# Optimization experiments

Measured on AMD Instinct MI355X. Metric: run time of the kernel, lower is better.

Reference implementation:

```python
import jax, jax.numpy as jnp
import numpy as np

B, NG, C, H = 16, 1024, 768, 12
CAP = 16  # fixed routing capacity in gpu_pair (8 box slots from 0 up, 8 cls slots from 15 down)


def layernorm(x, g, b, eps=1e-5):
    m = x.mean(-1, keepdims=True)
    v = jnp.mean((x - m) ** 2, axis=-1, keepdims=True)
    return (x - m) * jax.lax.rsqrt(v + eps) * g + b


def setup_inputs() -> dict:
    key = jax.random.key(0)
    ks = jax.random.split(key, 8)
    s = 0.02
    return {
        "general_token": jax.random.normal(ks[0], (B, NG, C), jnp.float32),
        "cls_token": jax.random.normal(ks[1], (B, 1, C), jnp.float32),
        "box_token": jax.random.normal(ks[2], (B, 1, C), jnp.float32),
        "w_qkv": jax.random.normal(ks[3], (3 * C, C), jnp.float32) * s,
        "w_proj": jax.random.normal(ks[4], (C, C), jnp.float32) * s,
        "b_proj": jnp.zeros((C,), jnp.float32),
        "gamma1": jnp.ones((C,), jnp.float32),
        "beta1": jnp.zeros((C,), jnp.float32),
    }


def _route(sum_a, is_box):
    """On-device replication of gpu_pair's serial CPU loop for slots 0..15.

    Tokens are processed in descending sum_attn order; box-preferred tokens fill
    slots 0,1,2,..., cls-preferred tokens fill slots 15,14,13,.... Each category's
    writer per slot is unique; on a box/cls collision the later (larger sorted
    position) write wins, matching the serial loop's overwrite semantics. Slots
    never written stay 0 (np.zeros init). Wrapped-around writes (rank >= 16) land
    outside slots 0..15 in the original and are irrelevant to the output.
    """
    ng = sum_a.shape[0]
    perm = jnp.argsort(-sum_a)                      # descending sort
    ib = is_box[perm]
    ibi = ib.astype(jnp.int32)
    box_rank = jnp.cumsum(ibi) - ibi                # exclusive prefix count of box tokens
    cls_rank = jnp.cumsum(1 - ibi) - (1 - ibi)      # exclusive prefix count of cls tokens
    j = jnp.arange(ng, dtype=jnp.int32)
    box_pos = jnp.where(ib & (box_rank < CAP), box_rank, CAP)
    cls_pos = jnp.where((~ib) & (cls_rank < CAP), (CAP - 1) - cls_rank, CAP)
    empty = jnp.full((CAP,), -1, jnp.int32)
    box_j = empty.at[box_pos].set(j, mode='drop')   # unique writer per slot
    cls_j = empty.at[cls_pos].set(j, mode='drop')
    win = jnp.maximum(box_j, cls_j)
    return jnp.where(win >= 0, perm[jnp.maximum(win, 0)], 0)


def reference(general_token, cls_token, box_token, w_qkv, w_proj, b_proj, gamma1, beta1):
    # cat order in torch: cat(cls, cat(box, general)) -> [cls, box, general]
    cat = jnp.concatenate([cls_token, box_token, general_token], axis=1)  # [B,N,C]
    Bq, N, Cq = cat.shape
    hd = Cq // H
    x = layernorm(cat, gamma1, beta1)
    qkv = (x @ w_qkv.T).reshape(Bq, N, 3, H, hd).transpose(2, 0, 3, 1, 4)
    q, k, v = qkv[0], qkv[1], qkv[2]
    attn = jnp.einsum('bhnd,bhmd->bhnm', q, k) * (hd ** -0.5)
    # raw scores between cls<->box zeroed BEFORE softmax (not -inf)
    attn = attn.at[:, :, 0, 1].set(0.0).at[:, :, 1, 0].set(0.0)
    attn = jax.nn.softmax(attn, axis=-1)
    out = jnp.einsum('bhnm,bhmd->bhnd', attn, v).transpose(0, 2, 1, 3).reshape(Bq, N, Cq)
    out = out @ w_proj.T + b_proj
    cat = cat + out  # residual (drop_path identity in eval)
    cls_t, box_t, gen = cat[:, 0:1], cat[:, 1:2], cat[:, 2:]
    cls_attn = attn[:, :, 0, 2:].mean(axis=1)  # [B, N-2]
    box_attn = attn[:, :, 1, 2:].mean(axis=1)
    idx = jax.vmap(_route)(cls_attn + box_attn, box_attn > cls_attn)  # [B,16]
    gathered = jnp.take_along_axis(gen, idx[:, :, None], axis=1)      # [B,16,C]
    cls_task_token = jnp.concatenate([cls_t, gathered[:, 0:8]], axis=1)   # [B,9,C]
    box_task_token = jnp.concatenate([box_t, gathered[:, 8:16]], axis=1)  # [B,9,C]
    return cls_task_token, box_task_token
```

## Files before the change

kernel.cpp:

```cpp
#include <hip/hip_runtime.h>
#include <math.h>

namespace {

constexpr int Bn = 16;
constexpr int NG = 1024;
constexpr int Cc = 768;
constexpr int Hh = 12;
constexpr int HD = 64;
constexpr int Nn = 1026;
constexpr int NR = 18;
constexpr int NPK = 1152;
constexpr int NCH = 8;

typedef __attribute__((ext_vector_type(8))) short short8;
typedef __attribute__((ext_vector_type(4))) float f32x4;

__device__ inline unsigned short f2bf(float f) {
  unsigned u = __float_as_uint(f);
  unsigned r = u + 0x7FFFu + ((u >> 16) & 1u);
  return (unsigned short)(r >> 16);
}

__global__ __launch_bounds__(256) void k_ln(
    const float* __restrict__ gen, const float* __restrict__ cls,
    const float* __restrict__ box, const float* __restrict__ gamma,
    const float* __restrict__ beta, float* __restrict__ x,
    unsigned short* __restrict__ xbf) {
  int blk = blockIdx.x;
  int b = blk / Nn, n = blk % Nn;
  const float* src = (n == 0) ? cls + (size_t)b * Cc
                   : (n == 1) ? box + (size_t)b * Cc
                              : gen + ((size_t)b * NG + (n - 2)) * Cc;
  int t = threadIdx.x;
  float v0 = src[t], v1 = src[t + 256], v2 = src[t + 512];
  __shared__ double red[8];
  double s = (double)v0 + (double)v1 + (double)v2;
  for (int o = 32; o > 0; o >>= 1) s += __shfl_down(s, o, 64);
  int wid = t >> 6, lid = t & 63;
  if (lid == 0) red[wid] = s;
  __syncthreads();
  if (t == 0) red[4] = (red[0] + red[1] + red[2] + red[3]) / Cc;
  __syncthreads();
  double mean = red[4];
  double d0 = (double)v0 - mean, d1 = (double)v1 - mean, d2 = (double)v2 - mean;
  double sq = d0 * d0 + d1 * d1 + d2 * d2;
  for (int o = 32; o > 0; o >>= 1) sq += __shfl_down(sq, o, 64);
  __syncthreads();
  if (lid == 0) red[wid] = sq;
  __syncthreads();
  if (t == 0) {
    double var = (red[0] + red[1] + red[2] + red[3]) / Cc;
    red[5] = 1.0 / sqrt(var + 1e-5);
  }
  __syncthreads();
  double rs = red[5];
  float* dst = x + ((size_t)b * Nn + n) * Cc;
  unsigned short* dbf = xbf + ((size_t)b * NPK + n) * Cc;
  float o0 = (float)(d0 * rs * (double)gamma[t]       + (double)beta[t]);
  float o1 = (float)(d1 * rs * (double)gamma[t + 256] + (double)beta[t + 256]);
  float o2 = (float)(d2 * rs * (double)gamma[t + 512] + (double)beta[t + 512]);
  dst[t] = o0; dst[t + 256] = o1; dst[t + 512] = o2;
  dbf[t] = f2bf(o0); dbf[t + 256] = f2bf(o1); dbf[t + 512] = f2bf(o2);
}

__global__ __launch_bounds__(256) void k_padzero(unsigned short* __restrict__ xbf) {
  constexpr int PERB = (NPK - Nn) * Cc / 2;
  int idx = blockIdx.x * 256 + threadIdx.x;
  int total = Bn * PERB;
  for (int i = idx; i < total; i += gridDim.x * 256) {
    int b = i / PERB, r = i % PERB;
    unsigned int* p = (unsigned int*)(xbf + ((size_t)b * NPK + Nn) * Cc);
    p[r] = 0u;
  }
}

__global__ __launch_bounds__(256) void k_xt(
    const unsigned short* __restrict__ xbf, unsigned short* __restrict__ xT) {
  int b = blockIdx.x, jt = blockIdx.y, ct = blockIdx.z;
  int j0 = jt * 64, c0 = ct * 64;
  __shared__ unsigned short ts[64][80];
  int t = threadIdx.x;
  #pragma unroll
  for (int l = 0; l < 2; l++) {
    int chunk = t + l * 256;
    int r = chunk >> 3, c8 = chunk & 7;
    uint4 v = *(const uint4*)(xbf + ((size_t)b * NPK + j0 + r) * Cc + c0 + c8 * 8);
    *(uint4*)&ts[r][c8 * 8] = v;
  }
  __syncthreads();
  #pragma unroll
  for (int l = 0; l < 2; l++) {
    int chunk = t + l * 256;
    int orow = chunk >> 3, j8 = chunk & 7;
    unsigned short tmp[8];
    #pragma unroll
    for (int i = 0; i < 8; i++) tmp[i] = ts[j8 * 8 + i][orow];
    *(uint4*)(xT + ((size_t)b * Cc + c0 + orow) * NPK + j0 + j8 * 8) = *(uint4*)tmp;
  }
}

__global__ __launch_bounds__(256) void k_wcvt(
    const float* __restrict__ wqkv, const float* __restrict__ wproj,
    unsigned short* __restrict__ wqb, unsigned short* __restrict__ wvb,
    unsigned short* __restrict__ wpb) {
  int i = (blockIdx.x * 256 + threadIdx.x) * 4;
  if (i >= Cc * Cc) return;
  const float* wq = wqkv;
  const float* wv = wqkv + (size_t)2 * Cc * Cc;
  float4 q = *(const float4*)(wq + i);
  float4 a = *(const float4*)(wv + i);
  float4 b = *(const float4*)(wproj + i);
  ushort4 oq, oa, ob;
  oq.x = f2bf(q.x); oq.y = f2bf(q.y); oq.z = f2bf(q.z); oq.w = f2bf(q.w);
  oa.x = f2bf(a.x); oa.y = f2bf(a.y); oa.z = f2bf(a.z); oa.w = f2bf(a.w);
  ob.x = f2bf(b.x); ob.y = f2bf(b.y); ob.z = f2bf(b.z); ob.w = f2bf(b.w);
  *(ushort4*)(wqb + i) = oq;
  *(ushort4*)(wvb + i) = oa;
  *(ushort4*)(wpb + i) = ob;
}

__global__ __launch_bounds__(256) void k_wkt(
    const float* __restrict__ wqkv, unsigned short* __restrict__ wkTb) {
  int rt = blockIdx.x, ct = blockIdx.y;
  __shared__ unsigned short ts[64][72];
  int t = threadIdx.x;
  const float* src = wqkv + (size_t)Cc * Cc;
  #pragma unroll
  for (int l = 0; l < 4; l++) {
    int idx = t + l * 256;
    int r = idx >> 4, c4 = idx & 15;
    float4 v = *(const float4*)(src + (size_t)(rt * 64 + r) * Cc + ct * 64 + c4 * 4);
    ts[r][c4 * 4 + 0] = f2bf(v.x); ts[r][c4 * 4 + 1] = f2bf(v.y);
    ts[r][c4 * 4 + 2] = f2bf(v.z); ts[r][c4 * 4 + 3] = f2bf(v.w);
  }
  __syncthreads();
  #pragma unroll
  for (int l = 0; l < 2; l++) {
    int idx = t + l * 256;
    int r2 = idx >> 3, j8 = idx & 7;
    unsigned short tmp[8];
    #pragma unroll
    for (int i = 0; i < 8; i++) tmp[i] = ts[j8 * 8 + i][r2];
    *(uint4*)(wkTb + (size_t)(ct * 64 + r2) * Cc + rt * 64 + j8 * 8) = *(uint4*)tmp;
  }
}

__global__ __launch_bounds__(256) void k_q01(
    const float* __restrict__ wqkv, const float* __restrict__ x,
    double* __restrict__ q01d) {
  int row = blockIdx.x;
  int b = row >> 1, i = row & 1;
  __shared__ float xl[Cc];
  const float* xr = x + ((size_t)b * Nn + i) * Cc;
  for (int c = threadIdx.x; c < Cc; c += 256) xl[c] = xr[c];
  __syncthreads();
  int w = threadIdx.x >> 6, lane = threadIdx.x & 63;
  int o = blockIdx.y * 4 + w;
  const float* wr = wqkv + (size_t)o * Cc + lane * 12;
  const float* xs = xl + lane * 12;
  double acc = 0;
  #pragma unroll
  for (int k = 0; k < 12; k++) acc += (double)wr[k] * (double)xs[k];
  for (int off = 32; off > 0; off >>= 1) acc += __shfl_down(acc, off, 64);
  if (lane == 0) q01d[(size_t)row * Cc + o] = acc;
}

__global__ __launch_bounds__(256) void k_u01(
    const float* __restrict__ wqkv, const double* __restrict__ q01d,
    double* __restrict__ u01d) {
  int blk = blockIdx.x;
  int h = blk % Hh; int i = (blk / Hh) & 1; int b = blk / (2 * Hh);
  __shared__ double qh[HD];
  const double* q = q01d + ((size_t)b * 2 + i) * Cc + h * HD;
  if (threadIdx.x < HD) qh[threadIdx.x] = q[threadIdx.x];
  __syncthreads();
  const float* wk = wqkv + (size_t)Cc * Cc;
  int c = blockIdx.y * 256 + threadIdx.x;
  double a0 = 0, a1 = 0, a2 = 0, a3 = 0;
  #pragma unroll 4
  for (int d = 0; d < HD; d += 4) {
    a0 += qh[d]     * (double)wk[(size_t)(h * HD + d) * Cc + c];
    a1 += qh[d + 1] * (double)wk[(size_t)(h * HD + d + 1) * Cc + c];
    a2 += qh[d + 2] * (double)wk[(size_t)(h * HD + d + 2) * Cc + c];
    a3 += qh[d + 3] * (double)wk[(size_t)(h * HD + d + 3) * Cc + c];
  }
  u01d[(((size_t)(b * 2 + i)) * Hh + h) * Cc + c] = (a0 + a1) + (a2 + a3);
}

__global__ __launch_bounds__(256) void k_rlogits(
    const double* __restrict__ u01d, const float* __restrict__ x,
    double* __restrict__ Ldp) {
  int b = blockIdx.x, jt = blockIdx.y, cch = blockIdx.z;
  int j0 = jt * 256;
  int t = threadIdx.x;
  int pl = t & 127;
  int g  = t >> 7;
  __shared__ float xtT[32][256];
  __shared__ double ut[24][32];
  double acc[12][2] = {};
  int cbase = cch * 96;
  for (int c0 = cbase; c0 < cbase + 96; c0 += 32) {
    {
      int j = j0 + t;
      if (j < Nn) {
        const float* xr = x + ((size_t)b * Nn + j) * Cc + c0;
        #pragma unroll
        for (int k = 0; k < 32; k += 4) {
          float4 v = *(const float4*)(xr + k);
          xtT[k][t] = v.x; xtT[k + 1][t] = v.y; xtT[k + 2][t] = v.z; xtT[k + 3][t] = v.w;
        }
      } else {
        for (int k = 0; k < 32; k++) xtT[k][t] = 0.f;
      }
    }
    for (int idx = t; idx < 24 * 32; idx += 256) {
      int r = idx >> 5, cc = idx & 31;
      ut[r][cc] = u01d[(((size_t)(b * 2 + (r / 12))) * Hh + (r % 12)) * Cc + c0 + cc];
    }
    __syncthreads();
    for (int cc = 0; cc < 32; cc++) {
      float2 xv = *(const float2*)&xtT[cc][pl * 2];
      double x0 = (double)xv.x, x1 = (double)xv.y;
      #pragma unroll
      for (int h = 0; h < 12; h++) {
        double uv = ut[g * 12 + h][cc];
        acc[h][0] += uv * x0;
        acc[h][1] += uv * x1;
      }
    }
    __syncthreads();
  }
  for (int h = 0; h < 12; h++) {
    #pragma unroll
    for (int k = 0; k < 2; k++) {
      int j = j0 + pl * 2 + k;
      if (j < Nn) {
        Ldp[(((size_t)cch * Bn + b) * 24 + g * 12 + h) * Nn + j] = acc[h][k] * 0.125;
      }
    }
  }
}

__global__ __launch_bounds__(256) void k_rsoftmax(
    const double* __restrict__ Ldp, double* __restrict__ Ld,
    unsigned short* __restrict__ Pb) {
  int blk = blockIdx.x;
  int h = blk % Hh; int i = (blk / Hh) & 1; int b = blk / (2 * Hh);
  double* row = Ld + (size_t)blk * Nn;
  unsigned short* prow = Pb + ((size_t)b * 216 + i * Hh + h) * NPK;
  int t = threadIdx.x;
  size_t poff = ((size_t)b * 24 + i * 12 + h) * Nn;
  constexpr size_t PSTRIDE = (size_t)Bn * 24 * Nn;
  double lv[5];
  int cnt = 0;
  double mx = -1e300;
  for (int j = t; j < Nn; j += 256) {
    double L = 0;
    #pragma unroll
    for (int p = 0; p < NCH; p++) L += Ldp[(size_t)p * PSTRIDE + poff + j];
    if (i == 0 && j == 1) L = 0.0;
    if (i == 1 && j == 0) L = 0.0;
    lv[cnt++] = L;
    mx = fmax(mx, L);
  }
  __shared__ double sd[256];
  sd[t] = mx; __syncthreads();
  for (int st = 128; st > 0; st >>= 1) { if (t < st) sd[t] = fmax(sd[t], sd[t + st]); __syncthreads(); }
  mx = sd[0]; __syncthreads();
  double sum = 0;
  for (int k = 0; k < cnt; k++) { lv[k] = exp(lv[k] - mx); sum += lv[k]; }
  sd[t] = sum; __syncthreads();
  for (int st = 128; st > 0; st >>= 1) { if (t < st) sd[t] += sd[t + st]; __syncthreads(); }
  double inv = 1.0 / sd[0];
  int k = 0;
  for (int j = t; j < Nn; j += 256) {
    double p = lv[k++] * inv;
    row[j] = p;
    prow[j] = f2bf((float)p);
  }
  for (int j = Nn + t; j < NPK; j += 256) prow[j] = 0;
}

__global__ __launch_bounds__(256) void k_rsums(
    const double* __restrict__ Ld, double* __restrict__ suma,
    double* __restrict__ diffd) {
  int b = blockIdx.x;
  for (int jg = threadIdx.x; jg < NG; jg += 256) {
    int j = jg + 2;
    double cs = 0, bs = 0;
    for (int h = 0; h < Hh; h++) {
      cs += Ld[(((size_t)(b * 2 + 0)) * Hh + h) * Nn + j];
      bs += Ld[(((size_t)(b * 2 + 1)) * Hh + h) * Nn + j];
    }
    cs /= 12.0; bs /= 12.0;
    suma[(size_t)b * NG + jg] = cs + bs;
    diffd[(size_t)b * NG + jg] = bs - cs;
  }
}

__global__ __launch_bounds__(256) void k_route(
    const double* __restrict__ suma, const double* __restrict__ diffd,
    int* __restrict__ rowcat) {
  int b = blockIdx.x, t = threadIdx.x;
  __shared__ double vals[NG];
  __shared__ unsigned char flags[NG];
  __shared__ double redv[4];
  __shared__ int redi[4];
  __shared__ int blist[16], clist[16];
  __shared__ double blv[16], clv[16];
  for (int j = t; j < NG; j += 256) {
    vals[j] = suma[(size_t)b * NG + j];
    flags[j] = diffd[(size_t)b * NG + j] > 0.0 ? 1 : 0;
  }
  __syncthreads();
  int half = t >> 7;
  int lt = t & 127;
  int wv = t >> 6;
  int lane = t & 63;
  for (int s = 0; s < 16; s++) {
    double bv = -1e300; int bi = 0x7fffffff;
    #pragma unroll
    for (int k = 0; k < 8; k++) {
      int j = lt * 8 + k;
      double v = vals[j];
      if (flags[j] == half && v > bv) { bv = v; bi = j; }
    }
    for (int off = 32; off > 0; off >>= 1) {
      double ov = __shfl_down(bv, off, 64);
      int oi = __shfl_down(bi, off, 64);
      if (ov > bv || (ov == bv && oi < bi)) { bv = ov; bi = oi; }
    }
    if (lane == 0) { redv[wv] = bv; redi[wv] = bi; }
    __syncthreads();
    if (lt == 0) {
      double v0 = redv[half * 2], v1 = redv[half * 2 + 1];
      int i0 = redi[half * 2], i1 = redi[half * 2 + 1];
      if (v1 > v0 || (v1 == v0 && i1 < i0)) { v0 = v1; i0 = i1; }
      int win = (v0 > -1e299) ? i0 : -1;
      if (half) { blist[s] = win; blv[s] = v0; }
      else      { clist[s] = win; clv[s] = v0; }
      if (win >= 0) vals[win] = -1e300;
    }
    __syncthreads();
  }
  if (t < 16) {
    int s = t;
    int bc = blist[s];
    int cl = clist[15 - s];
    double bvv = blv[s], cvv = clv[15 - s];
    int win;
    if (bc < 0 && cl < 0) win = -1;
    else if (bc < 0) win = cl;
    else if (cl < 0) win = bc;
    else {
      bool boxwins = (bvv < cvv) || (bvv == cvv && bc > cl);
      win = boxwins ? bc : cl;
    }
    int tok = (win >= 0) ? win : 0;
    rowcat[b * NR + 2 + s] = tok + 2;
  }
  if (t == 0) { rowcat[b * NR + 0] = 0; rowcat[b * NR + 1] = 1; }
}

__global__ __launch_bounds__(256) void k_qg_mfma(
    const unsigned short* __restrict__ xbf, const unsigned short* __restrict__ wqb,
    const int* __restrict__ rowcat, unsigned short* __restrict__ qb) {
  int mt = blockIdx.x, ng = blockIdx.y;
  int wid = threadIdx.x >> 6, lane = threadIdx.x & 63;
  int nt = ng * 4 + wid;
  int m = lane & 15, kg = lane >> 4;
  int rowi = mt * 16 + m;
  int b = rowi >> 4, s = rowi & 15;
  int tok = rowcat[b * NR + 2 + s];
  const unsigned short* abase = xbf + ((size_t)b * NPK + tok) * Cc + kg * 8;
  const unsigned short* bbase = wqb + (size_t)(nt * 16 + m) * Cc + kg * 8;
  f32x4 acc = {0, 0, 0, 0};
  for (int k0 = 0; k0 < Cc; k0 += 32) {
    short8 a = *(const short8*)(abase + k0);
    short8 bf = *(const short8*)(bbase + k0);
    acc = __builtin_amdgcn_mfma_f32_16x16x32_bf16(a, bf, acc, 0, 0, 0);
  }
  int c = nt * 16 + m;
  #pragma unroll
  for (int r = 0; r < 4; r++) {
    int rowo = mt * 16 + kg * 4 + r;
    qb[(size_t)rowo * Cc + c] = f2bf(acc[r]);
  }
}

__global__ __launch_bounds__(256) void k_ug_mfma(
    const unsigned short* __restrict__ qb, const unsigned short* __restrict__ wkTb,
    unsigned short* __restrict__ u16b) {
  int h = blockIdx.x, mt = blockIdx.y, ngz = blockIdx.z;
  int wid = threadIdx.x >> 6, lane = threadIdx.x & 63;
  int m = lane & 15, kg = lane >> 4;
  int rowi = mt * 16 + m;
  const unsigned short* abase = qb + (size_t)rowi * Cc + h * HD + kg * 8;
  f32x4 acc[4] = {{0,0,0,0},{0,0,0,0},{0,0,0,0},{0,0,0,0}};
  #pragma unroll
  for (int k0 = 0; k0 < HD; k0 += 32) {
    short8 a = *(const short8*)(abase + k0);
    #pragma unroll
    for (int t = 0; t < 4; t++) {
      int c = ngz * 256 + (wid * 4 + t) * 16 + m;
      short8 bf = *(const short8*)(wkTb + (size_t)c * Cc + h * HD + kg * 8 + k0);
      acc[t] = __builtin_amdgcn_mfma_f32_16x16x32_bf16(a, bf, acc[t], 0, 0, 0);
    }
  }
  #pragma unroll
  for (int t = 0; t < 4; t++) {
    int c = ngz * 256 + (wid * 4 + t) * 16 + m;
    #pragma unroll
    for (int r = 0; r < 4; r++) {
      int row = mt * 16 + kg * 4 + r;
      int b = row >> 4, s = row & 15;
      u16b[((size_t)b * 192 + s * Hh + h) * Cc + c] = f2bf(acc[t][r]);
    }
  }
}

__global__ __launch_bounds__(256) void k_glogits_mfma(
    const unsigned short* __restrict__ u16b, const unsigned short* __restrict__ xbf,
    float* __restrict__ S) {
  int b = blockIdx.x, mg = blockIdx.y, nz = blockIdx.z;
  __shared__ __align__(16) unsigned short Bs[2][128 * 32];
  int t = threadIdx.x, w = t >> 6, lane = t & 63;
  int wm = w >> 1, wn = w & 1;
  int m = lane & 15, kg = lane >> 4;
  int r0 = mg * 64 + wm * 32 + m;
  const unsigned short* a0p = u16b + ((size_t)b * 192 + r0) * Cc + kg * 8;
  const unsigned short* a1p = a0p + (size_t)16 * Cc;
  int scol = lane >> 2;
  int skp = (lane & 3) * 8;
  const unsigned short* gB0 = xbf + ((size_t)b * NPK + nz * 128 + w * 32 + scol) * Cc + skp;
  const unsigned short* gB1 = gB0 + (size_t)16 * Cc;
  int lo0 = (w * 32 + scol) * 32 + skp;
  int lo1 = lo0 + 16 * 32;
  constexpr int NIT = Cc / 32;
  short8 s0 = *(const short8*)(gB0);
  short8 s1 = *(const short8*)(gB1);
  *(short8*)&Bs[0][lo0] = s0;
  *(short8*)&Bs[0][lo1] = s1;
  __syncthreads();
  f32x4 acc[2][4] = {};
  for (int it = 0; it < NIT; it++) {
    int k0 = it * 32;
    int cur = it & 1;
    short8 n0, n1;
    if (it + 1 < NIT) {
      n0 = *(const short8*)(gB0 + k0 + 32);
      n1 = *(const short8*)(gB1 + k0 + 32);
    }
    short8 a0 = *(const short8*)(a0p + k0);
    short8 a1 = *(const short8*)(a1p + k0);
    #pragma unroll
    for (int tt = 0; tt < 4; tt++) {
      int col = wn * 64 + tt * 16 + m;
      short8 bf = *(const short8*)&Bs[cur][col * 32 + kg * 8];
      acc[0][tt] = __builtin_amdgcn_mfma_f32_16x16x32_bf16(a0, bf, acc[0][tt], 0, 0, 0);
      acc[1][tt] = __builtin_amdgcn_mfma_f32_16x16x32_bf16(a1, bf, acc[1][tt], 0, 0, 0);
    }
    if (it + 1 < NIT) {
      *(short8*)&Bs[cur ^ 1][lo0] = n0;
      *(short8*)&Bs[cur ^ 1][lo1] = n1;
    }
    __syncthreads();
  }
  #pragma unroll
  for (int mt = 0; mt < 2; mt++) {
    #pragma unroll
    for (int tt = 0; tt < 4; tt++) {
      int col = nz * 128 + wn * 64 + tt * 16 + m;
      #pragma unroll
      for (int r = 0; r < 4; r++) {
        int row = mg * 64 + wm * 32 + mt * 16 + kg * 4 + r;
        S[((size_t)b * 192 + row) * NPK + col] = acc[mt][tt][r] * 0.125f;
      }
    }
  }
}

__global__ __launch_bounds__(256) void k_gsoftmax(
    const float* __restrict__ S, unsigned short* __restrict__ Pb) {
  int blk = blockIdx.x;
  int b = blk / 192, r = blk % 192;
  const float* row = S + ((size_t)b * 192 + r) * NPK;
  unsigned short* prow = Pb + ((size_t)b * 216 + 24 + r) * NPK;
  int t = threadIdx.x;
  __shared__ float sd[256];
  float mx = -1e30f;
  for (int j = t; j < Nn; j += 256) mx = fmaxf(mx, row[j]);
  sd[t] = mx; __syncthreads();
  for (int st = 128; st > 0; st >>= 1) { if (t < st) sd[t] = fmaxf(sd[t], sd[t + st]); __syncthreads(); }
  mx = sd[0]; __syncthreads();
  float sum = 0;
  for (int j = t; j < Nn; j += 256) sum += __expf(row[j] - mx);
  sd[t] = sum; __syncthreads();
  for (int st = 128; st > 0; st >>= 1) { if (t < st) sd[t] += sd[t + st]; __syncthreads(); }
  float inv = 1.0f / sd[0];
  for (int j = t; j < NPK; j += 256) {
    prow[j] = (j < Nn) ? f2bf(__expf(row[j] - mx) * inv) : (unsigned short)0;
  }
}

__global__ __launch_bounds__(256) void k_wsum_mfma(
    const unsigned short* __restrict__ Pb, const unsigned short* __restrict__ xT,
    unsigned short* __restrict__ wsumb) {
  int b = blockIdx.x, mg = blockIdx.y, nz = blockIdx.z;
  __shared__ __align__(16) unsigned short Bs[2][128 * 32];
  int t = threadIdx.x, w = t >> 6, lane = t & 63;
  int wm = w >> 1, wn = w & 1;
  int m = lane & 15, kg = lane >> 4;
  int r0 = mg * 64 + wm * 32 + m;
  int rc0 = r0 < 216 ? r0 : 215;
  int rc1 = (r0 + 16) < 216 ? (r0 + 16) : 215;
  const unsigned short* a0p = Pb + ((size_t)b * 216 + rc0) * NPK + kg * 8;
  const unsigned short* a1p = Pb + ((size_t)b * 216 + rc1) * NPK + kg * 8;
  int scol = lane >> 2;
  int skp = (lane & 3) * 8;
  const unsigned short* gB0 = xT + ((size_t)b * Cc + nz * 128 + w * 32 + scol) * NPK + skp;
  const unsigned short* gB1 = gB0 + (size_t)16 * NPK;
  int lo0 = (w * 32 + scol) * 32 + skp;
  int lo1 = lo0 + 16 * 32;
  constexpr int NIT = NPK / 32;
  short8 s0 = *(const short8*)(gB0);
  short8 s1 = *(const short8*)(gB1);
  *(short8*)&Bs[0][lo0] = s0;
  *(short8*)&Bs[0][lo1] = s1;
  __syncthreads();
  f32x4 acc[2][4] = {};
  for (int it = 0; it < NIT; it++) {
    int k0 = it * 32;
    int cur = it & 1;
    short8 n0, n1;
    if (it + 1 < NIT) {
      n0 = *(const short8*)(gB0 + k0 + 32);
      n1 = *(const short8*)(gB1 + k0 + 32);
    }
    short8 a0 = *(const short8*)(a0p + k0);
    short8 a1 = *(const short8*)(a1p + k0);
    #pragma unroll
    for (int tt = 0; tt < 4; tt++) {
      int col = wn * 64 + tt * 16 + m;
      short8 bf = *(const short8*)&Bs[cur][col * 32 + kg * 8];
      acc[0][tt] = __builtin_amdgcn_mfma_f32_16x16x32_bf16(a0, bf, acc[0][tt], 0, 0, 0);
      acc[1][tt] = __builtin_amdgcn_mfma_f32_16x16x32_bf16(a1, bf, acc[1][tt], 0, 0, 0);
    }
    if (it + 1 < NIT) {
      *(short8*)&Bs[cur ^ 1][lo0] = n0;
      *(short8*)&Bs[cur ^ 1][lo1] = n1;
    }
    __syncthreads();
  }
  #pragma unroll
  for (int mt = 0; mt < 2; mt++) {
    #pragma unroll
    for (int tt = 0; tt < 4; tt++) {
      int col = nz * 128 + wn * 64 + tt * 16 + m;
      #pragma unroll
      for (int r = 0; r < 4; r++) {
        int row = mg * 64 + wm * 32 + mt * 16 + kg * 4 + r;
        if (row < 216) wsumb[((size_t)b * 216 + row) * Cc + col] = f2bf(acc[mt][tt][r]);
      }
    }
  }
}

__global__ __launch_bounds__(256) void k_attnout_mfma(
    const unsigned short* __restrict__ wsumb, const unsigned short* __restrict__ wvb,
    unsigned short* __restrict__ aob) {
  int h = blockIdx.x, mt = blockIdx.y;
  int wid = threadIdx.x >> 6, lane = threadIdx.x & 63;
  int m = lane & 15, kg = lane >> 4;
  int row = mt * 16 + m;
  int b = row / NR, i = row % NR;
  const unsigned short* abase = wsumb + ((size_t)b * 216 + i * 12 + h) * Cc + kg * 8;
  const unsigned short* bbase = wvb + (size_t)(h * HD + wid * 16 + m) * Cc + kg * 8;
  f32x4 acc = {0, 0, 0, 0};
  for (int k0 = 0; k0 < Cc; k0 += 32) {
    short8 a = *(const short8*)(abase + k0);
    short8 bf = *(const short8*)(bbase + k0);
    acc = __builtin_amdgcn_mfma_f32_16x16x32_bf16(a, bf, acc, 0, 0, 0);
  }
  #pragma unroll
  for (int r = 0; r < 4; r++) {
    int orow = mt * 16 + kg * 4 + r;
    int ocol = h * HD + wid * 16 + m;
    aob[(size_t)orow * Cc + ocol] = f2bf(acc[r]);
  }
}

__global__ __launch_bounds__(256) void k_proj_mfma(
    const unsigned short* __restrict__ aob, const unsigned short* __restrict__ wpb,
    const float* __restrict__ bproj, const int* __restrict__ rowcat,
    const float* __restrict__ gen, const float* __restrict__ cls,
    const float* __restrict__ box, float* __restrict__ out) {
  int mt = blockIdx.x, ng = blockIdx.y;
  int wid = threadIdx.x >> 6, lane = threadIdx.x & 63;
  int nt = ng * 4 + wid;
  int m = lane & 15, kg = lane >> 4;
  const unsigned short* abase = aob + (size_t)(mt * 16 + m) * Cc + kg * 8;
  const unsigned short* bbase = wpb + (size_t)(nt * 16 + m) * Cc + kg * 8;
  f32x4 acc = {0, 0, 0, 0};
  for (int k0 = 0; k0 < Cc; k0 += 32) {
    short8 a = *(const short8*)(abase + k0);
    short8 bf = *(const short8*)(bbase + k0);
    acc = __builtin_amdgcn_mfma_f32_16x16x32_bf16(a, bf, acc, 0, 0, 0);
  }
  int c = nt * 16 + m;
  float bp = bproj[c];
  #pragma unroll
  for (int r = 0; r < 4; r++) {
    int bi = mt * 16 + kg * 4 + r;
    int b = bi / NR, i = bi % NR;
    int tok = rowcat[b * NR + i];
    const float* src = (tok == 0) ? cls + (size_t)b * Cc
                     : (tok == 1) ? box + (size_t)b * Cc
                                  : gen + ((size_t)b * NG + tok - 2) * Cc;
    float val = acc[r] + bp + src[c];
    float* dst;
    if (i == 0)       dst = out + ((size_t)b * 9 + 0) * Cc;
    else if (i == 1)  dst = out + (size_t)Bn * 9 * Cc + ((size_t)b * 9 + 0) * Cc;
    else if (i < 10)  dst = out + ((size_t)b * 9 + (i - 1)) * Cc;
    else              dst = out + (size_t)Bn * 9 * Cc + ((size_t)b * 9 + (i - 9)) * Cc;
    dst[c] = val;
  }
}

}

extern "C" void kernel_launch(void* const* d_in, const int* in_sizes, int n_in,
                              void* d_out, int out_size, void* d_ws, size_t ws_size,
                              hipStream_t stream) {
  (void)in_sizes; (void)n_in; (void)out_size; (void)ws_size;
  const float* gen   = (const float*)d_in[0];
  const float* cls   = (const float*)d_in[1];
  const float* box   = (const float*)d_in[2];
  const float* wqkv  = (const float*)d_in[3];
  const float* wproj = (const float*)d_in[4];
  const float* bproj = (const float*)d_in[5];
  const float* gamma = (const float*)d_in[6];
  const float* beta  = (const float*)d_in[7];
  float* out = (float*)d_out;

  char* ws = (char*)d_ws;
  size_t off = 0;
  auto alloc = [&](size_t bytes) { void* p = ws + off; off += (bytes + 255) & ~(size_t)255; return p; };
  float* x             = (float*)alloc((size_t)Bn * Nn * Cc * 4);
  unsigned short* xbf  = (unsigned short*)alloc((size_t)Bn * NPK * Cc * 2);
  unsigned short* xT   = (unsigned short*)alloc((size_t)Bn * Cc * NPK * 2);
  unsigned short* qb   = (unsigned short*)alloc((size_t)256 * Cc * 2);
  unsigned short* u16b = (unsigned short*)alloc((size_t)Bn * 192 * Cc * 2);
  float* S             = (float*)alloc((size_t)Bn * 192 * NPK * 4);
  unsigned short* Pb   = (unsigned short*)alloc((size_t)Bn * 216 * NPK * 2);
  unsigned short* wsumb= (unsigned short*)alloc((size_t)Bn * 216 * Cc * 2);
  unsigned short* aob  = (unsigned short*)alloc((size_t)288 * Cc * 2);
  unsigned short* wqb  = (unsigned short*)alloc((size_t)Cc * Cc * 2);
  unsigned short* wvb  = (unsigned short*)alloc((size_t)Cc * Cc * 2);
  unsigned short* wpb  = (unsigned short*)alloc((size_t)Cc * Cc * 2);
  unsigned short* wkTb = (unsigned short*)alloc((size_t)Cc * Cc * 2);
  double* q01d         = (double*)alloc((size_t)Bn * 2 * Cc * 8);
  double* u01d         = (double*)alloc((size_t)Bn * 2 * Hh * Cc * 8);
  double* Ld           = (double*)alloc((size_t)Bn * 2 * Hh * Nn * 8);
  double* Ldp          = (double*)alloc((size_t)NCH * Bn * 24 * Nn * 8);
  double* suma         = (double*)alloc((size_t)Bn * NG * 8);
  double* diffd        = (double*)alloc((size_t)Bn * NG * 8);
  int* rowcat          = (int*)alloc((size_t)Bn * NR * 4);

  k_ln<<<Bn * Nn, 256, 0, stream>>>(gen, cls, box, gamma, beta, x, xbf);
  k_padzero<<<96, 256, 0, stream>>>(xbf);
  k_xt<<<dim3(Bn, NPK / 64, Cc / 64), 256, 0, stream>>>(xbf, xT);
  k_wcvt<<<(Cc * Cc / 4 + 255) / 256, 256, 0, stream>>>(wqkv, wproj, wqb, wvb, wpb);
  k_wkt<<<dim3(12, 12), 256, 0, stream>>>(wqkv, wkTb);
  k_q01<<<dim3(Bn * 2, 192), 256, 0, stream>>>(wqkv, x, q01d);
  k_u01<<<dim3(Bn * 2 * Hh, 3), 256, 0, stream>>>(wqkv, q01d, u01d);
  k_rlogits<<<dim3(Bn, 5, NCH), 256, 0, stream>>>(u01d, x, Ldp);
  k_rsoftmax<<<Bn * 2 * Hh, 256, 0, stream>>>(Ldp, Ld, Pb);
  k_rsums<<<Bn, 256, 0, stream>>>(Ld, suma, diffd);
  k_route<<<Bn, 256, 0, stream>>>(suma, diffd, rowcat);
  k_qg_mfma<<<dim3(16, 12), 256, 0, stream>>>(xbf, wqb, rowcat, qb);
  k_ug_mfma<<<dim3(Hh, 16, 3), 256, 0, stream>>>(qb, wkTb, u16b);
  k_glogits_mfma<<<dim3(Bn, 3, 9), 256, 0, stream>>>(u16b, xbf, S);
  k_gsoftmax<<<Bn * 192, 256, 0, stream>>>(S, Pb);
  k_wsum_mfma<<<dim3(Bn, 4, 6), 256, 0, stream>>>(Pb, xT, wsumb);
  k_attnout_mfma<<<dim3(Hh, 18), 256, 0, stream>>>(wsumb, wvb, aob);
  k_proj_mfma<<<dim3(18, 12), 256, 0, stream>>>(aob, wpb, bproj, rowcat, gen, cls, box, out);
}
```

Baseline: 300.4 us.

## Split routing logits: separate cls/box columns, retile general logits with fp32 partials

The two special key columns (cls/box) move into a small warp-reduction kernel, so the main routing-logits kernel tiles exactly 1024 general tokens without bounds checks, 4 outputs per thread and 24 channel chunks of 32. Partial sums are now stored as float instead of double, which halves partial-buffer traffic, and softmax adds the 24 partials back in double. This gives more blocks for parallelism and vectorized stores. The cost is more partials read in the softmax and some precision loss from fp32 partials, which could change the routing order near ties.

Measured after the change: 323.0 us. 1.08x slower.

```diff
diff --git a/kernel.cpp b/kernel.cpp
--- a/kernel.cpp
+++ b/kernel.cpp
@@ -11,7 +11,7 @@
 constexpr int Nn = 1026;
 constexpr int NR = 18;
 constexpr int NPK = 1152;
-constexpr int NCH = 8;
+constexpr int NCH = 24;
 
 typedef __attribute__((ext_vector_type(8))) short short8;
 typedef __attribute__((ext_vector_type(4))) float f32x4;
@@ -188,79 +188,106 @@
   u01d[(((size_t)(b * 2 + i)) * Hh + h) * Cc + c] = (a0 + a1) + (a2 + a3);
 }
 
+__global__ __launch_bounds__(256) void k_r01(
+    const double* __restrict__ u01d, const float* __restrict__ x,
+    double* __restrict__ Ld01) {
+  int b = blockIdx.x >> 1, i = blockIdx.x & 1;
+  int w = threadIdx.x >> 6, lane = threadIdx.x & 63;
+  for (int k = 0; k < 6; k++) {
+    int p = w * 6 + k;
+    int h = p >> 1, j = p & 1;
+    const double* u = u01d + (((size_t)(b * 2 + i)) * Hh + h) * Cc;
+    const float* xr = x + ((size_t)b * Nn + j) * Cc;
+    double acc = 0;
+    for (int c = lane; c < Cc; c += 64) acc += u[c] * (double)xr[c];
+    for (int off = 32; off > 0; off >>= 1) acc += __shfl_down(acc, off, 64);
+    if (lane == 0) Ld01[(((size_t)(b * 2 + i)) * Hh + h) * 2 + j] = acc * 0.125;
+  }
+}
+
 __global__ __launch_bounds__(256) void k_rlogits(
     const double* __restrict__ u01d, const float* __restrict__ x,
-    double* __restrict__ Ldp) {
+    float* __restrict__ Ldp) {
   int b = blockIdx.x, jt = blockIdx.y, cch = blockIdx.z;
-  int j0 = jt * 256;
+  int c0 = cch * 32;
   int t = threadIdx.x;
-  int pl = t & 127;
-  int g  = t >> 7;
-  __shared__ float xtT[32][256];
+  int w = t >> 6, lane = t & 63;
+  int g = w >> 1;
+  int pl = ((w & 1) << 6) + lane;
+  int jbase = jt * 512 + pl * 4;
   __shared__ double ut[24][32];
-  double acc[12][2] = {};
-  int cbase = cch * 96;
-  for (int c0 = cbase; c0 < cbase + 96; c0 += 32) {
-    {
-      int j = j0 + t;
-      if (j < Nn) {
-        const float* xr = x + ((size_t)b * Nn + j) * Cc + c0;
-        #pragma unroll
-        for (int k = 0; k < 32; k += 4) {
-          float4 v = *(const float4*)(xr + k);
-          xtT[k][t] = v.x; xtT[k + 1][t] = v.y; xtT[k + 2][t] = v.z; xtT[k + 3][t] = v.w;
-        }
-      } else {
-        for (int k = 0; k < 32; k++) xtT[k][t] = 0.f;
-      }
-    }
-    for (int idx = t; idx < 24 * 32; idx += 256) {
-      int r = idx >> 5, cc = idx & 31;
-      ut[r][cc] = u01d[(((size_t)(b * 2 + (r / 12))) * Hh + (r % 12)) * Cc + c0 + cc];
-    }
+  __shared__ float xtT[8][512];
+  #pragma unroll
+  for (int l = 0; l < 3; l++) {
+    int ii = t + l * 256;
+    int row = ii >> 5, cc = ii & 31;
+    int ig = row / 12, hh = row % 12;
+    ut[row][cc] = u01d[(((size_t)(b * 2 + ig)) * Hh + hh) * Cc + c0 + cc];
+  }
+  double acc[12][4] = {};
+  for (int s = 0; s < 4; s++) {
     __syncthreads();
-    for (int cc = 0; cc < 32; cc++) {
-      float2 xv = *(const float2*)&xtT[cc][pl * 2];
-      double x0 = (double)xv.x, x1 = (double)xv.y;
+    #pragma unroll
+    for (int l = 0; l < 4; l++) {
+      int idx = t + l * 256;
+      int jl = idx >> 1, half = idx & 1;
+      const float* xr = x + ((size_t)b * Nn + 2 + jt * 512 + jl) * Cc + c0 + s * 8 + half * 4;
+      float4 v = *(const float4*)xr;
+      xtT[half * 4 + 0][jl] = v.x;
+      xtT[half * 4 + 1][jl] = v.y;
+      xtT[half * 4 + 2][jl] = v.z;
+      xtT[half * 4 + 3][jl] = v.w;
+    }
+    __syncthreads();
+    #pragma unroll
+    for (int cc8 = 0; cc8 < 8; cc8++) {
+      int cc = s * 8 + cc8;
+      float4 xv = *(const float4*)&xtT[cc8][pl * 4];
+      double x0 = (double)xv.x, x1 = (double)xv.y, x2 = (double)xv.z, x3 = (double)xv.w;
       #pragma unroll
       for (int h = 0; h < 12; h++) {
         double uv = ut[g * 12 + h][cc];
         acc[h][0] += uv * x0;
         acc[h][1] += uv * x1;
+        acc[h][2] += uv * x2;
+        acc[h][3] += uv * x3;
       }
     }
-    __syncthreads();
   }
   for (int h = 0; h < 12; h++) {
-    #pragma unroll
-    for (int k = 0; k < 2; k++) {
-      int j = j0 + pl * 2 + k;
-      if (j < Nn) {
-        Ldp[(((size_t)cch * Bn + b) * 24 + g * 12 + h) * Nn + j] = acc[h][k] * 0.125;
-      }
-    }
+    float4 o;
+    o.x = (float)(acc[h][0] * 0.125);
+    o.y = (float)(acc[h][1] * 0.125);
+    o.z = (float)(acc[h][2] * 0.125);
+    o.w = (float)(acc[h][3] * 0.125);
+    *(float4*)&Ldp[(((size_t)cch * Bn + b) * 24 + g * 12 + h) * 1024 + jbase] = o;
   }
 }
 
 __global__ __launch_bounds__(256) void k_rsoftmax(
-    const double* __restrict__ Ldp, double* __restrict__ Ld,
-    unsigned short* __restrict__ Pb) {
+    const float* __restrict__ Ldp, const double* __restrict__ Ld01,
+    double* __restrict__ Ld, unsigned short* __restrict__ Pb) {
   int blk = blockIdx.x;
   int h = blk % Hh; int i = (blk / Hh) & 1; int b = blk / (2 * Hh);
   double* row = Ld + (size_t)blk * Nn;
   unsigned short* prow = Pb + ((size_t)b * 216 + i * Hh + h) * NPK;
   int t = threadIdx.x;
-  size_t poff = ((size_t)b * 24 + i * 12 + h) * Nn;
-  constexpr size_t PSTRIDE = (size_t)Bn * 24 * Nn;
+  size_t poff = ((size_t)b * 24 + i * 12 + h) * 1024;
+  constexpr size_t PSTRIDE = (size_t)Bn * 24 * 1024;
   double lv[5];
   int cnt = 0;
   double mx = -1e300;
   for (int j = t; j < Nn; j += 256) {
-    double L = 0;
-    #pragma unroll
-    for (int p = 0; p < NCH; p++) L += Ldp[(size_t)p * PSTRIDE + poff + j];
-    if (i == 0 && j == 1) L = 0.0;
-    if (i == 1 && j == 0) L = 0.0;
+    double L;
+    if (j < 2) {
+      L = Ld01[(((size_t)(b * 2 + i)) * Hh + h) * 2 + j];
+      if (i == 0 && j == 1) L = 0.0;
+      if (i == 1 && j == 0) L = 0.0;
+    } else {
+      L = 0;
+      #pragma unroll
+      for (int p = 0; p < NCH; p++) L += (double)Ldp[(size_t)p * PSTRIDE + poff + (j - 2)];
+    }
     lv[cnt++] = L;
     mx = fmax(mx, L);
   }
@@ -663,7 +690,8 @@
   double* q01d         = (double*)alloc((size_t)Bn * 2 * Cc * 8);
   double* u01d         = (double*)alloc((size_t)Bn * 2 * Hh * Cc * 8);
   double* Ld           = (double*)alloc((size_t)Bn * 2 * Hh * Nn * 8);
-  double* Ldp          = (double*)alloc((size_t)NCH * Bn * 24 * Nn * 8);
+  double* Ld01         = (double*)alloc((size_t)Bn * 2 * Hh * 2 * 8);
+  float* Ldp           = (float*)alloc((size_t)NCH * Bn * 24 * 1024 * 4);
   double* suma         = (double*)alloc((size_t)Bn * NG * 8);
   double* diffd        = (double*)alloc((size_t)Bn * NG * 8);
   int* rowcat          = (int*)alloc((size_t)Bn * NR * 4);
@@ -675,8 +703,9 @@
   k_wkt<<<dim3(12, 12), 256, 0, stream>>>(wqkv, wkTb);
   k_q01<<<dim3(Bn * 2, 192), 256, 0, stream>>>(wqkv, x, q01d);
   k_u01<<<dim3(Bn * 2 * Hh, 3), 256, 0, stream>>>(wqkv, q01d, u01d);
-  k_rlogits<<<dim3(Bn, 5, NCH), 256, 0, stream>>>(u01d, x, Ldp);
-  k_rsoftmax<<<Bn * 2 * Hh, 256, 0, stream>>>(Ldp, Ld, Pb);
+  k_r01<<<Bn * 2, 256, 0, stream>>>(u01d, x, Ld01);
+  k_rlogits<<<dim3(Bn, 2, NCH), 256, 0, stream>>>(u01d, x, Ldp);
+  k_rsoftmax<<<Bn * 2 * Hh, 256, 0, stream>>>(Ldp, Ld01, Ld, Pb);
   k_rsums<<<Bn, 256, 0, stream>>>(Ld, suma, diffd);
   k_route<<<Bn, 256, 0, stream>>>(suma, diffd, rowcat);
   k_qg_mfma<<<dim3(16, 12), 256, 0, stream>>>(xbf, wqb, rowcat, qb);
```
